# Kernel optimization log

Hardware: AMD Instinct MI355X
Metric: run time of the kernel (lower is better)

Reference implementation:

```python
import jax, jax.numpy as jnp
import numpy as np

B, T, D, H = 4, 1024, 1024, 16  # batch, seq, model dim (named head_size in source), n_heads


def setup_inputs() -> dict:
    key = jax.random.key(0)
    ks = jax.random.split(key, 12)
    s = 0.02
    x = jax.random.normal(ks[0], (B, T, D), jnp.float32)
    x1 = jax.random.normal(ks[1], (1,), jnp.float32)  # unused by module
    x2 = jax.random.normal(ks[2], (1,), jnp.float32)  # unused by module
    # bool mask, True = masked out; causal upper-triangular as typical usage
    attn_mask = jnp.triu(jnp.ones((T, T), dtype=bool), k=1)
    Wk = jax.random.normal(ks[3], (D, D), jnp.float32) * s
    bk = jax.random.normal(ks[4], (D,), jnp.float32) * s
    Wq = jax.random.normal(ks[5], (D, D), jnp.float32) * s
    bq = jax.random.normal(ks[6], (D,), jnp.float32) * s
    Wv = jax.random.normal(ks[7], (D, D), jnp.float32) * s
    bv = jax.random.normal(ks[8], (D,), jnp.float32) * s
    Wp = jax.random.normal(ks[9], (D, D), jnp.float32) * s
    bp = jax.random.normal(ks[10], (D,), jnp.float32) * s
    return {"x": x, "x1": x1, "x2": x2, "attn_mask": attn_mask,
            "Wk": Wk, "bk": bk, "Wq": Wq, "bq": bq,
            "Wv": Wv, "bv": bv, "Wp": Wp, "bp": bp}


def reference(x, x1, x2, attn_mask, Wk, bk, Wq, bq, Wv, bv, Wp, bp):
    b, t, c = x.shape
    n_heads = H
    hd = c // n_heads
    # torch nn.Linear: y = x @ W.T + b
    k = (x @ Wk.T + bk).reshape(b, t, n_heads, hd)
    q = (x @ Wq.T + bq).reshape(b, t, n_heads, hd)
    v = (x @ Wv.T + bv).reshape(b, t, n_heads, hd)
    scores = jnp.einsum('bkhi,bqhi->bkqh', k, q)  # [B,T(k),T(q),H]
    # mask BEFORE scaling (as in source; -inf is scale-invariant)
    scores = jnp.where(attn_mask[None, :t, :t, None], -jnp.inf, scores)
    scores = scores / jnp.sqrt(jnp.asarray(c, scores.dtype))  # scale by full model dim (source quirk)
    weights = jax.nn.softmax(scores, axis=2)  # softmax over QUERY axis (source quirk)
    out = jnp.einsum('bkqh,bqhj->bkhj', weights, v).reshape(b, t, c)
    out = out @ Wp.T + bp  # dropout p=0 -> identity
    return (out, weights)
```

## Files before the change

### kernel.cpp

```cpp
#include <hip/hip_runtime.h>
#include <cstdint>


typedef __bf16 bf16x8 __attribute__((ext_vector_type(8)));
typedef float  f32x4  __attribute__((ext_vector_type(4)));
typedef unsigned int u32x4 __attribute__((ext_vector_type(4)));
using u16 = unsigned short;
using u32 = unsigned int;

__device__ __forceinline__ float bf2f(u16 u) {
  union { u32 u; float f; } x; x.u = ((u32)u) << 16; return x.f;
}
__device__ __forceinline__ u16 f2bf(float f) {
  union { float f; u32 u; } x; x.f = f;
  u32 u = x.u;
  return (u16)((u + 0x7fffu + ((u >> 16) & 1u)) >> 16);
}

#define GLL(g, s) __builtin_amdgcn_global_load_lds(                      \
    (const __attribute__((address_space(1))) u32*)(g),                   \
    (__attribute__((address_space(3))) u32*)(s), 16, 0, 0)

__global__ __launch_bounds__(256) void cvt_all(const float* __restrict__ x,
                                               const float* __restrict__ wk,
                                               const float* __restrict__ wq,
                                               const float* __restrict__ wv,
                                               const float* __restrict__ wp,
                                               uint2* __restrict__ out,
                                               const float* __restrict__ bkp,
                                               const float* __restrict__ bqp,
                                               float* __restrict__ bqkv) {
  if (blockIdx.x >= 8192) {
    int t2 = (blockIdx.x - 8192) * 256 + threadIdx.x;
    const float* s = (t2 < 1024) ? bkp : bqp;
    bqkv[t2] = s[t2 & 1023];
    return;
  }
  int i = blockIdx.x * 256 + threadIdx.x;
  const float* src; int off;
  if (i < 1048576) { src = x; off = i; }
  else {
    int j = i - 1048576; int w = j >> 18; off = j & 262143;
    src = (w == 0) ? wk : (w == 1) ? wq : (w == 2) ? wv : wp;
  }
  f32x4 v = __builtin_nontemporal_load((const f32x4*)(src + off * 4));
  uint2 o;
  o.x = (u32)f2bf(v[0]) | ((u32)f2bf(v[1]) << 16);
  o.y = (u32)f2bf(v[2]) | ((u32)f2bf(v[3]) << 16);
  out[i] = o;
}

__global__ __launch_bounds__(256) void gemm_qkvt(
    const u16* __restrict__ xb, const u16* __restrict__ wkb,
    const float* __restrict__ bkq, const float* __restrict__ bv,
    u16* __restrict__ kq, u16* __restrict__ vt)
{
  const int z  = blockIdx.z;
  const int n0 = blockIdx.x * 128;
  const u16 *A, *B; u16* C; const float* bias;
  int m0; bool rowBias;
  if (z < 2) {
    m0 = blockIdx.y * 128;
    A = xb; B = wkb + z * 1048576; C = kq + (size_t)z * 4194304;
    bias = bkq + z * 1024; rowBias = false;
  } else {
    const int b = blockIdx.y >> 3;
    m0 = (blockIdx.y & 7) * 128;
    A = wkb + 2 * 1048576; B = xb + (size_t)b * 1048576; C = vt + (size_t)b * 1048576;
    bias = bv; rowBias = true;
  }

  __shared__ __align__(16) u16 As[128 * 32];
  __shared__ __align__(16) u16 Bs[128 * 32];

  const int t    = threadIdx.x;
  const int wave = t >> 6;
  const int lane = t & 63;

  const int r0 = (wave * 2 + 0) * 16 + (lane >> 2);
  const int r1 = (wave * 2 + 1) * 16 + (lane >> 2);
  const int cl = (lane & 3) * 8;
  const u16* aG0 = A + (size_t)(m0 + r0) * 1024 + cl;
  const u16* aG1 = A + (size_t)(m0 + r1) * 1024 + cl;
  const u16* bG0 = B + (size_t)(n0 + r0) * 1024 + cl;
  const u16* bG1 = B + (size_t)(n0 + r1) * 1024 + cl;
  u16* asD0 = As + (wave * 2 + 0) * 512;
  u16* asD1 = As + (wave * 2 + 1) * 512;
  u16* bsD0 = Bs + (wave * 2 + 0) * 512;
  u16* bsD1 = Bs + (wave * 2 + 1) * 512;

  const int wm = (wave >> 1) << 6;
  const int wn = (wave & 1) << 6;
  const int lr = lane & 15;
  const int lk = (lane >> 4) << 3;

  f32x4 acc[4][4];
  const f32x4 fzero = {0.f, 0.f, 0.f, 0.f};
#pragma unroll
  for (int i = 0; i < 4; i++)
#pragma unroll
    for (int j = 0; j < 4; j++) acc[i][j] = fzero;

  for (int k0 = 0; k0 < 1024; k0 += 32) {
    __syncthreads();
    GLL(aG0 + k0, asD0);
    GLL(aG1 + k0, asD1);
    GLL(bG0 + k0, bsD0);
    GLL(bG1 + k0, bsD1);
    __syncthreads();

    bf16x8 af[4], bf[4];
#pragma unroll
    for (int mi = 0; mi < 4; mi++)
      af[mi] = *(const bf16x8*)&As[(wm + mi * 16 + lr) * 32 + lk];
#pragma unroll
    for (int ni = 0; ni < 4; ni++)
      bf[ni] = *(const bf16x8*)&Bs[(wn + ni * 16 + lr) * 32 + lk];
#pragma unroll
    for (int mi = 0; mi < 4; mi++)
#pragma unroll
      for (int ni = 0; ni < 4; ni++)
        acc[mi][ni] = __builtin_amdgcn_mfma_f32_16x16x32_bf16(af[mi], bf[ni], acc[mi][ni], 0, 0, 0);
  }

  const int cr = (lane >> 4) << 2;
  const int cc = lane & 15;
#pragma unroll
  for (int mi = 0; mi < 4; mi++) {
#pragma unroll
    for (int ni = 0; ni < 4; ni++) {
      int gn = n0 + wn + ni * 16 + cc;
      float bcol = rowBias ? 0.f : bias[gn];
      int gm = m0 + wm + mi * 16 + cr;
#pragma unroll
      for (int r = 0; r < 4; r++) {
        float badd = rowBias ? bias[gm + r] : bcol;
        C[(size_t)(gm + r) * 1024 + gn] = f2bf(acc[mi][ni][r] + badd);
      }
    }
  }
}

__global__ __launch_bounds__(256, 2) void fused_attn(
    const u16* __restrict__ kq,
    const u16* __restrict__ vt,
    u16* __restrict__ sc, u16* __restrict__ attn, float* __restrict__ lbuf)
{
  const int xx = blockIdx.x, yy = blockIdx.y;
  int kbv = (xx + yy) & 7;
  if (yy & 32) kbv = 7 - kbv;
  const int kb = kbv;
  const int bh = yy;
  const int b  = bh >> 4, h = bh & 15;
  const int k0 = kb << 7;

  __shared__ __align__(16) u16 Kl[128 * 72];
  __shared__ __align__(16) u16 QV[128 * 72];
  __shared__ __align__(16) u16 Pl[128 * 136];
  __shared__ float l_sm[2][128];

  const int t    = threadIdx.x;
  const int wave = t >> 6, lane = t & 63;
  const int wm = (wave >> 1) << 6, wn = (wave & 1) << 6;
  const int lr = lane & 15, lk = (lane >> 4) << 3;
  const int cr = (lane >> 4) << 2, cc = lane & 15;

  {
    const int r = t >> 1, cb = (t & 1) << 5;
    const u16* g = kq + (size_t)(b * 1024 + k0 + r) * 1024 + h * 64 + cb;
    u16* d = Kl + r * 72 + cb;
#pragma unroll
    for (int i = 0; i < 4; i++)
      *(uint4*)(d + i * 8) = *(const uint4*)(g + i * 8);
  }

  const u16* qbase = kq + 4194304 + (size_t)(b * 1024) * 1024 + h * 64;
  const u16* vbase = vt + (size_t)(bh * 64) * 1024;

  f32x4 oacc[2][4];
  const f32x4 fz = {0.f, 0.f, 0.f, 0.f};
#pragma unroll
  for (int i = 0; i < 2; i++)
#pragma unroll
    for (int j = 0; j < 4; j++) oacc[i][j] = fz;
  float lsum[4][4] = {};

  const int qr = t >> 1, qcb = (t & 1) << 5;
  const int vr = t >> 2, vcb = (t & 3) << 5;

  for (int tq = 0; tq <= kb; tq++) {
    const int q0 = tq << 7;
    uint4 qreg[4], vreg[4];
    const u16* qg = qbase + (size_t)(q0 + qr) * 1024 + qcb;
    const u16* vg = vbase + (size_t)vr * 1024 + q0 + vcb;
#pragma unroll
    for (int i = 0; i < 4; i++) qreg[i] = *(const uint4*)(qg + i * 8);
#pragma unroll
    for (int i = 0; i < 4; i++) vreg[i] = *(const uint4*)(vg + i * 8);

    __syncthreads();
    {
      u16* d = QV + qr * 72 + qcb;
#pragma unroll
      for (int i = 0; i < 4; i++) *(uint4*)(d + i * 8) = qreg[i];
    }
    __syncthreads();

    f32x4 sacc[4][4];
#pragma unroll
    for (int i = 0; i < 4; i++)
#pragma unroll
      for (int j = 0; j < 4; j++) sacc[i][j] = fz;
#pragma unroll
    for (int ks = 0; ks < 2; ks++) {
      bf16x8 af[4], bf[4];
#pragma unroll
      for (int mi = 0; mi < 4; mi++)
        af[mi] = *(const bf16x8*)&Kl[(wm + mi * 16 + lr) * 72 + ks * 32 + lk];
#pragma unroll
      for (int ni = 0; ni < 4; ni++)
        bf[ni] = *(const bf16x8*)&QV[(wn + ni * 16 + lr) * 72 + ks * 32 + lk];
#pragma unroll
      for (int mi = 0; mi < 4; mi++)
#pragma unroll
        for (int ni = 0; ni < 4; ni++)
          sacc[mi][ni] = __builtin_amdgcn_mfma_f32_16x16x32_bf16(af[mi], bf[ni], sacc[mi][ni], 0, 0, 0);
    }
    __syncthreads();

#pragma unroll
    for (int mi = 0; mi < 4; mi++) {
#pragma unroll
      for (int ni = 0; ni < 4; ni++) {
        const int col = wn + ni * 16 + cc;
#pragma unroll
        for (int r = 0; r < 4; r++) {
          const int row = wm + mi * 16 + cr + r;
          bool valid = (q0 + col) <= (k0 + row);
          float e = valid ? __expf(sacc[mi][ni][r] * 0.03125f) : 0.f;
          lsum[mi][r] += e;
          Pl[row * 136 + col] = f2bf(e);
        }
      }
    }
    {
      u16* d = QV + vr * 136 + vcb;
#pragma unroll
      for (int i = 0; i < 4; i++) *(uint4*)(d + i * 8) = vreg[i];
    }
    __syncthreads();

#pragma unroll
    for (int ks = 0; ks < 4; ks++) {
      bf16x8 pa[2], vb[4];
#pragma unroll
      for (int mi = 0; mi < 2; mi++)
        pa[mi] = *(const bf16x8*)&Pl[(wave * 32 + mi * 16 + lr) * 136 + ks * 32 + lk];
#pragma unroll
      for (int ni = 0; ni < 4; ni++)
        vb[ni] = *(const bf16x8*)&QV[(ni * 16 + lr) * 136 + ks * 32 + lk];
#pragma unroll
      for (int mi = 0; mi < 2; mi++)
#pragma unroll
        for (int ni = 0; ni < 4; ni++)
          oacc[mi][ni] = __builtin_amdgcn_mfma_f32_16x16x32_bf16(pa[mi], vb[ni], oacc[mi][ni], 0, 0, 0);
    }
    {
      const int rr = t >> 4, cp = (t & 15) << 3;
      u16* g = sc + ((size_t)bh << 20) + (size_t)(k0 + rr) * 1024 + q0 + cp;
      const u16* s = Pl + rr * 136 + cp;
#pragma unroll
      for (int i = 0; i < 8; i++) {
        u32x4 v = *(const u32x4*)(s + i * 16 * 136);
        __builtin_nontemporal_store(v, (u32x4*)(g + (size_t)(i * 16) * 1024));
      }
    }
  }

#pragma unroll
  for (int mi = 0; mi < 4; mi++)
#pragma unroll
    for (int r = 0; r < 4; r++) {
      float v = lsum[mi][r];
#pragma unroll
      for (int o = 1; o < 16; o <<= 1) v += __shfl_xor(v, o, 64);
      lsum[mi][r] = v;
    }
  __syncthreads();
  if ((lane & 15) == 0) {
#pragma unroll
    for (int mi = 0; mi < 4; mi++)
#pragma unroll
      for (int r = 0; r < 4; r++)
        l_sm[wave & 1][wm + mi * 16 + cr + r] = lsum[mi][r];
  }
  __syncthreads();
  if (t < 128)
    lbuf[(size_t)bh * 1024 + k0 + t] = l_sm[0][t] + l_sm[1][t];

#pragma unroll
  for (int mi = 0; mi < 2; mi++) {
#pragma unroll
    for (int r = 0; r < 4; r++) {
      const int row = wave * 32 + mi * 16 + cr + r;
      const float rinv = 1.f / (l_sm[0][row] + l_sm[1][row]);
#pragma unroll
      for (int ni = 0; ni < 4; ni++)
        attn[(size_t)(b * 1024 + k0 + row) * 1024 + h * 64 + ni * 16 + cc] =
            f2bf(oacc[mi][ni][r] * rinv);
    }
  }
}

__global__ __launch_bounds__(256) void expand_proj(
    const u16* __restrict__ sw, const float* __restrict__ lbuf, float* __restrict__ out_w,
    const u16* __restrict__ A, const u16* __restrict__ Bw,
    const float* __restrict__ bias, float* __restrict__ Cout)
{
  __shared__ __align__(16) u32 shm[16 * 577];

  if (blockIdx.x < 256) {
    const int bx = blockIdx.x;
    const int m0 = (bx >> 3) * 128;
    const int n0 = (bx & 7) * 128;

    u16* AsB = (u16*)shm;
    u16* BsB = AsB + 4096;

    const int t    = threadIdx.x;
    const int wave = t >> 6;
    const int lane = t & 63;

    const int r0 = (wave * 2 + 0) * 16 + (lane >> 2);
    const int r1 = (wave * 2 + 1) * 16 + (lane >> 2);
    const int cl = (lane & 3) * 8;
    const u16* aG0 = A + (size_t)(m0 + r0) * 1024 + cl;
    const u16* aG1 = A + (size_t)(m0 + r1) * 1024 + cl;
    const u16* bG0 = Bw + (size_t)(n0 + r0) * 1024 + cl;
    const u16* bG1 = Bw + (size_t)(n0 + r1) * 1024 + cl;
    u16* asD0 = AsB + (wave * 2 + 0) * 512;
    u16* asD1 = AsB + (wave * 2 + 1) * 512;
    u16* bsD0 = BsB + (wave * 2 + 0) * 512;
    u16* bsD1 = BsB + (wave * 2 + 1) * 512;

    const int wm = (wave >> 1) << 6;
    const int wn = (wave & 1) << 6;
    const int lr = lane & 15;
    const int lk = (lane >> 4) << 3;

    f32x4 acc[4][4];
    const f32x4 fzero = {0.f, 0.f, 0.f, 0.f};
#pragma unroll
    for (int i = 0; i < 4; i++)
#pragma unroll
      for (int j = 0; j < 4; j++) acc[i][j] = fzero;

    for (int k0 = 0; k0 < 1024; k0 += 32) {
      __syncthreads();
      GLL(aG0 + k0, asD0);
      GLL(aG1 + k0, asD1);
      GLL(bG0 + k0, bsD0);
      GLL(bG1 + k0, bsD1);
      __syncthreads();

      bf16x8 af[4], bf[4];
#pragma unroll
      for (int mi = 0; mi < 4; mi++)
        af[mi] = *(const bf16x8*)&AsB[(wm + mi * 16 + lr) * 32 + lk];
#pragma unroll
      for (int ni = 0; ni < 4; ni++)
        bf[ni] = *(const bf16x8*)&BsB[(wn + ni * 16 + lr) * 32 + lk];
#pragma unroll
      for (int mi = 0; mi < 4; mi++)
#pragma unroll
        for (int ni = 0; ni < 4; ni++)
          acc[mi][ni] = __builtin_amdgcn_mfma_f32_16x16x32_bf16(af[mi], bf[ni], acc[mi][ni], 0, 0, 0);
    }

    const int cr = (lane >> 4) << 2;
    const int cc = lane & 15;
#pragma unroll
    for (int mi = 0; mi < 4; mi++) {
#pragma unroll
      for (int ni = 0; ni < 4; ni++) {
        int gn = n0 + wn + ni * 16 + cc;
        float bv = bias[gn];
        int gm = m0 + wm + mi * 16 + cr;
#pragma unroll
        for (int r = 0; r < 4; r++)
          Cout[(size_t)(gm + r) * 1024 + gn] = acc[mi][ni][r] + bv;
      }
    }
    return;
  }

  const int bk   = blockIdx.x - 256;
  const int b    = bk >> 10, k = bk & 1023;
  const int t    = threadIdx.x;
  const int wave = t >> 6;
  const int lane = t & 63;
  const int qb   = lane << 4;

#pragma unroll
  for (int i = 0; i < 4; i++) {
    const int h = wave * 4 + i;
    const float rinv = 1.f / lbuf[(size_t)(b * 16 + h) * 1024 + k];
    const u16* row = sw + (((size_t)(b * 16 + h)) << 20) + ((size_t)k << 10);

    union { u32x4 d; u16 s[8]; } a0, a1;
    if (qb <= k) {
      a0.d = __builtin_nontemporal_load((const u32x4*)(row + qb));
      a1.d = __builtin_nontemporal_load((const u32x4*)(row + qb + 8));
    } else {
      a0.d = (u32x4){0, 0, 0, 0};
      a1.d = (u32x4){0, 0, 0, 0};
    }

    u16 outp[16];
#pragma unroll
    for (int j = 0; j < 16; j++) {
      u16 raw = (j < 8) ? a0.s[j] : a1.s[j - 8];
      float e = ((qb + j) <= k) ? bf2f(raw) * rinv : 0.f;
      outp[j] = f2bf(e);
    }

    u32* run = &shm[h * 577 + lane * 9];
#pragma unroll
    for (int j = 0; j < 8; j++) run[j] = (u32)outp[2 * j] | ((u32)outp[2 * j + 1] << 16);
  }
  __syncthreads();

  f32x4* o = (f32x4*)(out_w + ((size_t)bk << 14));
#pragma unroll
  for (int p = 0; p < 16; p++) {
    const int q    = p * 64 + (t >> 2);
    const int Lr   = q >> 4;
    const int pr   = (q & 15) >> 1;
    const int half = (q & 1) << 4;
    f32x4 v;
#pragma unroll
    for (int j = 0; j < 4; j++) {
      const int hh = (t & 3) * 4 + j;
      u32 packed = shm[hh * 577 + Lr * 9 + pr];
      v[j] = bf2f((u16)(packed >> half));
    }
    __builtin_nontemporal_store(v, o + p * 256 + t);
  }
}

extern "C" void kernel_launch(void* const* d_in, const int* in_sizes, int n_in,
                              void* d_out, int out_size, void* d_ws, size_t ws_size,
                              hipStream_t stream) {
  const float* x  = (const float*)d_in[0];
  const float* Wk = (const float*)d_in[4];
  const float* bk = (const float*)d_in[5];
  const float* Wq = (const float*)d_in[6];
  const float* bq = (const float*)d_in[7];
  const float* Wv = (const float*)d_in[8];
  const float* bv = (const float*)d_in[9];
  const float* Wp = (const float*)d_in[10];
  const float* bp = (const float*)d_in[11];

  float* out   = (float*)d_out;
  float* out_w = out + 4194304;

  u16* ws   = (u16*)d_ws;
  u16* xb   = ws;
  u16* wkb  = xb  + 4194304;
  u16* kbuf = wkb + 4194304;
  u16* vt   = kbuf + 12582912;
  u16* attn = vt   + 4194304;
  u16* sc   = attn + 4194304;
  float* bqkv = (float*)(sc + 67108864);
  float* lbuf = bqkv + 3072;

  cvt_all<<<8200, 256, 0, stream>>>(x, Wk, Wq, Wv, Wp, (uint2*)ws, bk, bq, bqkv);

  gemm_qkvt<<<dim3(8, 32, 3), 256, 0, stream>>>(xb, wkb, bqkv, bv, kbuf, vt);

  fused_attn<<<dim3(8, 64), 256, 0, stream>>>(kbuf, vt, sc, attn, lbuf);

  expand_proj<<<4352, 256, 0, stream>>>(sc, lbuf, out_w,
                                        attn, wkb + 3145728, bp, out);
}
```

Before: 461.2 us.

## Load Q and V fragments directly from global memory, drop LDS staging

Removes the shared-memory staging buffer for Q and V tiles. MFMA operand fragments are now read straight from global memory (relying on L2/L1 cache), which eliminates two barriers per iteration and frees LDS, so occupancy is raised to 3 blocks per CU. The causal mask check is also split so that only the diagonal tile evaluates it. The cost is more global load traffic per wave, with uncoalesced 16-byte row-strided accesses and latency that is no longer hidden by register prefetch.

```diff
diff --git a/kernel.cpp b/kernel.cpp
--- a/kernel.cpp
+++ b/kernel.cpp
@@ -141,7 +141,7 @@
   }
 }
 
-__global__ __launch_bounds__(256, 2) void fused_attn(
+__global__ __launch_bounds__(256, 3) void fused_attn(
     const u16* __restrict__ kq,
     const u16* __restrict__ vt,
     u16* __restrict__ sc, u16* __restrict__ attn, float* __restrict__ lbuf)
@@ -155,7 +155,6 @@
   const int k0 = kb << 7;
 
   __shared__ __align__(16) u16 Kl[128 * 72];
-  __shared__ __align__(16) u16 QV[128 * 72];
   __shared__ __align__(16) u16 Pl[128 * 136];
   __shared__ float l_sm[2][128];
 
@@ -173,6 +172,7 @@
     for (int i = 0; i < 4; i++)
       *(uint4*)(d + i * 8) = *(const uint4*)(g + i * 8);
   }
+  __syncthreads();
 
   const u16* qbase = kq + 4194304 + (size_t)(b * 1024) * 1024 + h * 64;
   const u16* vbase = vt + (size_t)(bh * 64) * 1024;
@@ -185,26 +185,8 @@
     for (int j = 0; j < 4; j++) oacc[i][j] = fz;
   float lsum[4][4] = {};
 
-  const int qr = t >> 1, qcb = (t & 1) << 5;
-  const int vr = t >> 2, vcb = (t & 3) << 5;
-
   for (int tq = 0; tq <= kb; tq++) {
     const int q0 = tq << 7;
-    uint4 qreg[4], vreg[4];
-    const u16* qg = qbase + (size_t)(q0 + qr) * 1024 + qcb;
-    const u16* vg = vbase + (size_t)vr * 1024 + q0 + vcb;
-#pragma unroll
-    for (int i = 0; i < 4; i++) qreg[i] = *(const uint4*)(qg + i * 8);
-#pragma unroll
-    for (int i = 0; i < 4; i++) vreg[i] = *(const uint4*)(vg + i * 8);
-
-    __syncthreads();
-    {
-      u16* d = QV + qr * 72 + qcb;
-#pragma unroll
-      for (int i = 0; i < 4; i++) *(uint4*)(d + i * 8) = qreg[i];
-    }
-    __syncthreads();
 
     f32x4 sacc[4][4];
 #pragma unroll
@@ -219,34 +201,45 @@
         af[mi] = *(const bf16x8*)&Kl[(wm + mi * 16 + lr) * 72 + ks * 32 + lk];
 #pragma unroll
       for (int ni = 0; ni < 4; ni++)
-        bf[ni] = *(const bf16x8*)&QV[(wn + ni * 16 + lr) * 72 + ks * 32 + lk];
+        bf[ni] = *(const bf16x8*)(qbase + (size_t)(q0 + wn + ni * 16 + lr) * 1024 + ks * 32 + lk);
 #pragma unroll
       for (int mi = 0; mi < 4; mi++)
 #pragma unroll
         for (int ni = 0; ni < 4; ni++)
           sacc[mi][ni] = __builtin_amdgcn_mfma_f32_16x16x32_bf16(af[mi], bf[ni], sacc[mi][ni], 0, 0, 0);
     }
+
     __syncthreads();
 
-#pragma unroll
-    for (int mi = 0; mi < 4; mi++) {
-#pragma unroll
-      for (int ni = 0; ni < 4; ni++) {
-        const int col = wn + ni * 16 + cc;
-#pragma unroll
-        for (int r = 0; r < 4; r++) {
-          const int row = wm + mi * 16 + cr + r;
-          bool valid = (q0 + col) <= (k0 + row);
-          float e = valid ? __expf(sacc[mi][ni][r] * 0.03125f) : 0.f;
-          lsum[mi][r] += e;
-          Pl[row * 136 + col] = f2bf(e);
+    if (tq < kb) {
+#pragma unroll
+      for (int mi = 0; mi < 4; mi++)
+#pragma unroll
+        for (int ni = 0; ni < 4; ni++) {
+          const int col = wn + ni * 16 + cc;
+#pragma unroll
+          for (int r = 0; r < 4; r++) {
+            const int row = wm + mi * 16 + cr + r;
+            float e = __expf(sacc[mi][ni][r] * 0.03125f);
+            lsum[mi][r] += e;
+            Pl[row * 136 + col] = f2bf(e);
+          }
         }
-      }
-    }
-    {
-      u16* d = QV + vr * 136 + vcb;
-#pragma unroll
-      for (int i = 0; i < 4; i++) *(uint4*)(d + i * 8) = vreg[i];
+    } else {
+#pragma unroll
+      for (int mi = 0; mi < 4; mi++)
+#pragma unroll
+        for (int ni = 0; ni < 4; ni++) {
+          const int col = wn + ni * 16 + cc;
+#pragma unroll
+          for (int r = 0; r < 4; r++) {
+            const int row = wm + mi * 16 + cr + r;
+            bool valid = col <= row;
+            float e = valid ? __expf(sacc[mi][ni][r] * 0.03125f) : 0.f;
+            lsum[mi][r] += e;
+            Pl[row * 136 + col] = f2bf(e);
+          }
+        }
     }
     __syncthreads();
 
@@ -258,7 +251,7 @@
         pa[mi] = *(const bf16x8*)&Pl[(wave * 32 + mi * 16 + lr) * 136 + ks * 32 + lk];
 #pragma unroll
       for (int ni = 0; ni < 4; ni++)
-        vb[ni] = *(const bf16x8*)&QV[(ni * 16 + lr) * 136 + ks * 32 + lk];
+        vb[ni] = *(const bf16x8*)(vbase + (size_t)(ni * 16 + lr) * 1024 + q0 + ks * 32 + lk);
 #pragma unroll
       for (int mi = 0; mi < 2; mi++)
 #pragma unroll
```

Measured after the change: 462.0 us. Within noise of the previous version (+0.2%).
